# Performance work log

Hardware: AMD Instinct MI355X
Metric: run time of the kernel (lower is better)

Reference implementation:

```python
import jax, jax.numpy as jnp
import numpy as np

GROUPS = 32
EPS = 1e-5


def group_norm(x, scale, bias):
    # x: [B,H,W,C]; stats over (H, W, channels-within-group)
    B, H, W, C = x.shape
    xg = x.reshape(B, H, W, GROUPS, C // GROUPS)
    mean = xg.mean(axis=(1, 2, 4), keepdims=True)
    var = xg.var(axis=(1, 2, 4), keepdims=True)
    xn = ((xg - mean) * jax.lax.rsqrt(var + EPS)).reshape(B, H, W, C)
    return xn * scale + bias


def conv1x1(x, w, b):
    # 1x1 conv == per-pixel matmul; w: [C_in, C_out]
    return jnp.einsum('bhwc,cd->bhwd', x, w) + b


def setup_inputs() -> dict:
    key = jax.random.key(0)
    ks = jax.random.split(key, 10)
    B, H, W, C = 8, 64, 64, 512
    bound = np.sqrt(3.0 / C)  # variance_scaling(1.0, fan_in, uniform)
    x = jax.random.normal(ks[0], (B, H, W, C), dtype=jnp.float32)
    wq = jax.random.uniform(ks[1], (C, C), jnp.float32, -bound, bound)
    wk = jax.random.uniform(ks[2], (C, C), jnp.float32, -bound, bound)
    wv = jax.random.uniform(ks[3], (C, C), jnp.float32, -bound, bound)
    wp = jnp.zeros((C, C), jnp.float32)  # proj_out init scale=0.0
    bq = jnp.zeros((C,), jnp.float32)
    bk = jnp.zeros((C,), jnp.float32)
    bv = jnp.zeros((C,), jnp.float32)
    bp = jnp.zeros((C,), jnp.float32)
    gn_scale = jnp.ones((C,), jnp.float32)
    gn_bias = jnp.zeros((C,), jnp.float32)
    return {"x": x, "wq": wq, "bq": bq, "wk": wk, "bk": bk, "wv": wv,
            "bv": bv, "wp": wp, "bp": bp, "gn_scale": gn_scale, "gn_bias": gn_bias}


def reference(x, wq, bq, wk, bk, wv, bv, wp, bp, gn_scale, gn_bias):
    B, H, W, C = x.shape
    h = group_norm(x, gn_scale, gn_bias)
    q = conv1x1(h, wq, bq).reshape(B, H * W, C)
    k = conv1x1(h, wk, bk).reshape(B, H * W, C)
    v = conv1x1(h, wv, bv).reshape(B, H * W, C)
    # contraction over spatial dim j=H*W -> channel attention [B, C, C]
    attn = jnp.einsum('bji,bjk->bik', q, k)
    attn = jax.nn.softmax(attn, axis=-1)
    h = jnp.einsum('bij,bkj->bik', v, attn)  # [B, HW, C]
    h = h.reshape(B, H, W, C)
    h = conv1x1(h, wp, bp)
    return x + h
```

## Files before the change

kernel.cpp:

```cpp
#include <hip/hip_runtime.h>
#include <hip/hip_bf16.h>


using bf16   = __bf16;
using bf16x8 = __attribute__((ext_vector_type(8))) __bf16;
using bf16x4 = __attribute__((ext_vector_type(4))) __bf16;
using f32x4  = __attribute__((ext_vector_type(4))) float;

#define DI __device__ __forceinline__

DI void gload16(const bf16* g, bf16* l) {
  __builtin_amdgcn_global_load_lds(
      (const __attribute__((address_space(1))) void*)g,
      (__attribute__((address_space(3))) void*)l, 16, 0, 0);
}

DI void gemm128_core(const bf16* __restrict__ A, long lda,
                     const bf16* __restrict__ B, long ldb,
                     int ksteps, bf16* As, bf16* Bs, f32x4 acc[4][4]) {
  const int tid  = threadIdx.x;
  const int lane = tid & 63;
  const int w    = tid >> 6;
  const int lr   = lane & 15;
  const int lk   = (lane >> 4) * 8;
  const int wr   = (w >> 1) * 64;
  const int wc   = (w & 1) * 64;
  const int sw   = (lr & 7) << 3;

  const int  srow = lane >> 3;
  const int  ssw  = ((lane & 7) ^ srow) << 3;
  const bf16* ga = A + (long)(w * 8 + srow) * lda + ssw;
  const bf16* gb = B + (long)(w * 8 + srow) * ldb + ssw;
  bf16* lA = As + w * 512;
  bf16* lB = Bs + w * 512;

  for (int kt = 0; kt < ksteps; ++kt) {
#pragma unroll
    for (int c = 0; c < 4; ++c) {
      gload16(ga + (long)c * 32 * lda, lA + c * 2048);
      gload16(gb + (long)c * 32 * ldb, lB + c * 2048);
    }
    ga += 64; gb += 64;
    __syncthreads();
#pragma unroll
    for (int kk = 0; kk < 2; ++kk) {
      bf16x8 af[4], bfr[4];
#pragma unroll
      for (int i = 0; i < 4; ++i)
        af[i] = *(const bf16x8*)(As + (wr + i * 16 + lr) * 64 + ((kk * 32 + lk) ^ sw));
#pragma unroll
      for (int i = 0; i < 4; ++i)
        bfr[i] = *(const bf16x8*)(Bs + (wc + i * 16 + lr) * 64 + ((kk * 32 + lk) ^ sw));
#pragma unroll
      for (int i = 0; i < 4; ++i)
#pragma unroll
        for (int j = 0; j < 4; ++j)
          acc[i][j] = __builtin_amdgcn_mfma_f32_16x16x32_bf16(af[i], bfr[j], acc[i][j], 0, 0, 0);
    }
    __syncthreads();
  }
}

DI void gemm128x64_core(const bf16* __restrict__ A, long lda,
                        const bf16* __restrict__ B, long ldb,
                        int ksteps, bf16* As, bf16* Bs, f32x4 acc[4][2]) {
  const int tid  = threadIdx.x;
  const int lane = tid & 63;
  const int w    = tid >> 6;
  const int lr   = lane & 15;
  const int lk   = (lane >> 4) * 8;
  const int wr   = (w >> 1) * 64;
  const int wc   = (w & 1) * 32;
  const int sw   = (lr & 7) << 3;

  const int  srow = lane >> 3;
  const int  ssw  = ((lane & 7) ^ srow) << 3;
  const bf16* ga = A + (long)(w * 8 + srow) * lda + ssw;
  const bf16* gb = B + (long)(w * 8 + srow) * ldb + ssw;
  bf16* lA = As + w * 512;
  bf16* lB = Bs + w * 512;

  for (int kt = 0; kt < ksteps; ++kt) {
#pragma unroll
    for (int c = 0; c < 4; ++c)
      gload16(ga + (long)c * 32 * lda, lA + c * 2048);
#pragma unroll
    for (int c = 0; c < 2; ++c)
      gload16(gb + (long)c * 32 * ldb, lB + c * 2048);
    ga += 64; gb += 64;
    __syncthreads();
#pragma unroll
    for (int kk = 0; kk < 2; ++kk) {
      bf16x8 af[4], bfr[2];
#pragma unroll
      for (int i = 0; i < 4; ++i)
        af[i] = *(const bf16x8*)(As + (wr + i * 16 + lr) * 64 + ((kk * 32 + lk) ^ sw));
#pragma unroll
      for (int j = 0; j < 2; ++j)
        bfr[j] = *(const bf16x8*)(Bs + (wc + j * 16 + lr) * 64 + ((kk * 32 + lk) ^ sw));
#pragma unroll
      for (int i = 0; i < 4; ++i)
#pragma unroll
        for (int j = 0; j < 2; ++j)
          acc[i][j] = __builtin_amdgcn_mfma_f32_16x16x32_bf16(af[i], bfr[j], acc[i][j], 0, 0, 0);
    }
    __syncthreads();
  }
}

DI void gemm64_core(const bf16* __restrict__ A, long lda,
                    const bf16* __restrict__ B, long ldb,
                    int ksteps, bf16* As, bf16* Bs, f32x4 acc[2][2]) {
  const int tid  = threadIdx.x;
  const int lane = tid & 63;
  const int w    = tid >> 6;
  const int lr   = lane & 15;
  const int lk   = (lane >> 4) * 8;
  const int wr   = (w >> 1) * 32;
  const int wc   = (w & 1) * 32;
  const int sw   = (lr & 7) << 3;

  const int  srow = lane >> 3;
  const int  ssw  = ((lane & 7) ^ srow) << 3;
  const bf16* ga = A + (long)(w * 8 + srow) * lda + ssw;
  const bf16* gb = B + (long)(w * 8 + srow) * ldb + ssw;
  bf16* lA = As + w * 512;
  bf16* lB = Bs + w * 512;

  for (int kt = 0; kt < ksteps; ++kt) {
#pragma unroll
    for (int c = 0; c < 2; ++c) {
      gload16(ga + (long)c * 32 * lda, lA + c * 2048);
      gload16(gb + (long)c * 32 * ldb, lB + c * 2048);
    }
    ga += 64; gb += 64;
    __syncthreads();
#pragma unroll
    for (int kk = 0; kk < 2; ++kk) {
      bf16x8 af[2], bfr[2];
#pragma unroll
      for (int i = 0; i < 2; ++i)
        af[i] = *(const bf16x8*)(As + (wr + i * 16 + lr) * 64 + ((kk * 32 + lk) ^ sw));
#pragma unroll
      for (int i = 0; i < 2; ++i)
        bfr[i] = *(const bf16x8*)(Bs + (wc + i * 16 + lr) * 64 + ((kk * 32 + lk) ^ sw));
#pragma unroll
      for (int i = 0; i < 2; ++i)
#pragma unroll
        for (int j = 0; j < 2; ++j)
          acc[i][j] = __builtin_amdgcn_mfma_f32_16x16x32_bf16(af[i], bfr[j], acc[i][j], 0, 0, 0);
    }
    __syncthreads();
  }
}

__global__ __launch_bounds__(256) void k_prep(const float* __restrict__ x,
                                              const float* __restrict__ wq,
                                              const float* __restrict__ wk,
                                              const float* __restrict__ wv,
                                              const float* __restrict__ wp,
                                              bf16* __restrict__ WT,
                                              bf16* __restrict__ wvb,
                                              float* __restrict__ s,
                                              float2* __restrict__ stats) {
  __shared__ float shm[1056];
  const int tid = threadIdx.x;
  const int bx = blockIdx.x;
  if (bx < 256) {
    const int b = bx >> 5, g = bx & 31;
    const float* base = x + (size_t)b * 4096 * 512 + g * 16;
    float sm = 0.f, ss = 0.f;
    for (int it = 0; it < 64; ++it) {
      const int idx = it * 256 + tid;
      const int p = idx >> 2, c4 = (idx & 3) * 4;
      float4 v = *(const float4*)(base + (size_t)p * 512 + c4);
      sm += v.x + v.y + v.z + v.w;
      ss += v.x * v.x + v.y * v.y + v.z * v.z + v.w * v.w;
    }
    float* rs = shm; float* rss = shm + 256;
    rs[tid] = sm; rss[tid] = ss; __syncthreads();
    for (int off = 128; off; off >>= 1) {
      if (tid < off) { rs[tid] += rs[tid + off]; rss[tid] += rss[tid + off]; }
      __syncthreads();
    }
    if (tid == 0) {
      float mean = rs[0] * (1.f / 65536.f);
      float var  = rss[0] * (1.f / 65536.f) - mean * mean;
      stats[bx] = float2{mean, rsqrtf(var + 1e-5f)};
    }
  } else {
    const int r = bx - 256;
    const int z = r >> 8;
    const int r2 = r & 255;
    const int bxx = r2 & 15, byy = r2 >> 4;
    const int tx = tid & 31, ty = tid >> 5;
    const float* src = (z == 0) ? wq : (z == 1) ? wk : (z == 2) ? wv : wp;
    const int n0 = bxx * 32, k0 = byy * 32;
    if (z == 0 && byy == 0) s[bxx * 256 + tid] = 0.f;
#pragma unroll
    for (int j = 0; j < 4; ++j) {
      const float v = src[(size_t)(k0 + ty + j * 8) * 512 + n0 + tx];
      shm[(ty + j * 8) * 33 + tx] = v;
      if (z == 2) wvb[(size_t)(k0 + ty + j * 8) * 512 + n0 + tx] = (bf16)v;
    }
    __syncthreads();
#pragma unroll
    for (int j = 0; j < 4; ++j)
      WT[(size_t)(z * 512 + n0 + ty + j * 8) * 512 + k0 + tx] = (bf16)shm[tx * 33 + ty + j * 8];
  }
}

__global__ __launch_bounds__(256) void k_gnapply_t(const float* __restrict__ x,
                                                   const float2* __restrict__ stats,
                                                   const float* __restrict__ gns,
                                                   const float* __restrict__ gnb,
                                                   bf16* __restrict__ Hn,
                                                   bf16* __restrict__ HnT,
                                                   float* __restrict__ s) {
  __shared__ bf16 tile[64 * 516];
  __shared__ float cs[512];
  const int tid = threadIdx.x;
  const int blk = blockIdx.x;
  const int b = blk >> 6, p0 = (blk & 63) * 64;
  cs[tid] = 0.f; cs[tid + 256] = 0.f;
  __syncthreads();

  const int c4 = (tid & 127) * 4;
  const int hi = tid >> 7;
  const float2 st = stats[b * 32 + (c4 >> 4)];
  const float4 sc = *(const float4*)(gns + c4);
  const float4 bi = *(const float4*)(gnb + c4);
  float a0 = 0.f, a1 = 0.f, a2 = 0.f, a3 = 0.f;
  for (int i = 0; i < 32; ++i) {
    const int px = i * 2 + hi;
    const float4 xv = *(const float4*)(x + ((size_t)(b * 4096 + p0 + px)) * 512 + c4);
    const float h0 = (xv.x - st.x) * st.y * sc.x + bi.x;
    const float h1 = (xv.y - st.x) * st.y * sc.y + bi.y;
    const float h2 = (xv.z - st.x) * st.y * sc.z + bi.z;
    const float h3 = (xv.w - st.x) * st.y * sc.w + bi.w;
    a0 += h0; a1 += h1; a2 += h2; a3 += h3;
    bf16x4 hv;
    hv[0] = (bf16)h0; hv[1] = (bf16)h1; hv[2] = (bf16)h2; hv[3] = (bf16)h3;
    *(bf16x4*)(Hn + ((size_t)(b * 4096 + p0 + px)) * 512 + c4) = hv;
    *(bf16x4*)(tile + px * 516 + c4) = hv;
  }
  atomicAdd(&cs[c4 + 0], a0); atomicAdd(&cs[c4 + 1], a1);
  atomicAdd(&cs[c4 + 2], a2); atomicAdd(&cs[c4 + 3], a3);
  __syncthreads();
  atomicAdd(s + b * 512 + tid, cs[tid]);
  atomicAdd(s + b * 512 + 256 + tid, cs[tid + 256]);

  for (int cg = 0; cg < 16; ++cg) {
    const int c  = cg * 32 + (tid >> 3);
    const int so = (tid & 7) * 8;
    bf16x8 pk;
#pragma unroll
    for (int k = 0; k < 8; ++k) pk[k] = tile[(so + k) * 516 + c];
    *(bf16x8*)(HnT + ((size_t)(b * 512 + c)) * 4096 + p0 + so) = pk;
  }
}

__global__ __launch_bounds__(256) void k_gram(const bf16* __restrict__ HnT,
                                              bf16* __restrict__ part) {
  __shared__ bf16 As[128 * 64], Bs[128 * 64];
  const int Lb = blockIdx.x;
  const int b  = Lb & 7;
  const int idx = Lb >> 3;
  const int sp = idx & 3;
  const int t  = idx >> 2;
  const int m0 = (int)((0x3221110000ull >> (4 * t)) & 15) * 128;
  const int n0 = (int)((0x3323213210ull >> (4 * t)) & 15) * 128;
  f32x4 acc[4][4];
#pragma unroll
  for (int i = 0; i < 4; ++i)
#pragma unroll
    for (int j = 0; j < 4; ++j) acc[i][j] = (f32x4){0.f, 0.f, 0.f, 0.f};
  const bf16* A = HnT + ((size_t)b * 512 + m0) * 4096 + sp * 1024;
  const bf16* B = HnT + ((size_t)b * 512 + n0) * 4096 + sp * 1024;
  gemm128_core(A, 4096, B, 4096, 16, As, Bs, acc);

  const int lane = threadIdx.x & 63, w = threadIdx.x >> 6;
  const int wr = (w >> 1) * 64, wc = (w & 1) * 64;
  const int rr = (lane >> 4) * 4, cc = lane & 15;
  bf16* dst = part + (size_t)(sp * 8 + b) * 262144;
#pragma unroll
  for (int i = 0; i < 4; ++i) {
#pragma unroll
    for (int j = 0; j < 4; ++j) {
      const int gm = m0 + wr + i * 16 + rr;
      const int gn = n0 + wc + j * 16 + cc;
      bf16* p = dst + (size_t)gm * 512 + gn;
      p[0]    = (bf16)acc[i][j][0];
      p[512]  = (bf16)acc[i][j][1];
      p[1024] = (bf16)acc[i][j][2];
      p[1536] = (bf16)acc[i][j][3];
      if (m0 != n0) {
        bf16x4 pk;
        pk[0] = (bf16)acc[i][j][0]; pk[1] = (bf16)acc[i][j][1];
        pk[2] = (bf16)acc[i][j][2]; pk[3] = (bf16)acc[i][j][3];
        *(bf16x4*)(dst + (size_t)gn * 512 + gm) = pk;
      }
    }
  }
}

__global__ __launch_bounds__(256) void k_gsumv(const bf16* __restrict__ part,
                                               bf16* __restrict__ G,
                                               const bf16* __restrict__ WT,
                                               const float* __restrict__ s,
                                               float* __restrict__ uq,
                                               float* __restrict__ vkv) {
  const int bx = blockIdx.x, tid = threadIdx.x;
  if (bx < 2048) {
    const size_t S8 = (size_t)8 * 262144;
    const size_t i4 = ((size_t)bx * 256 + tid) * 4;
    const bf16x4 a = *(const bf16x4*)(part + i4);
    const bf16x4 c = *(const bf16x4*)(part + i4 + S8);
    const bf16x4 d = *(const bf16x4*)(part + i4 + 2 * S8);
    const bf16x4 e = *(const bf16x4*)(part + i4 + 3 * S8);
    bf16x4 o;
#pragma unroll
    for (int j = 0; j < 4; ++j)
      o[j] = (bf16)((float)a[j] + (float)c[j] + (float)d[j] + (float)e[j]);
    *(bf16x4*)(G + i4) = o;
  } else {
    const int z = bx - 2048;
    const int which = z >> 3, b = z & 7;
    const float* sv = s + b * 512;
    for (int o = tid; o < 512; o += 256) {
      const bf16* row = WT + ((size_t)(which * 512 + o)) * 512;
      float acc = 0.f;
      for (int c = 0; c < 512; c += 8) {
        bf16x8 v = *(const bf16x8*)(row + c);
        const float4 s0 = *(const float4*)(sv + c);
        const float4 s1 = *(const float4*)(sv + c + 4);
        acc += (float)v[0] * s0.x + (float)v[1] * s0.y + (float)v[2] * s0.z +
               (float)v[3] * s0.w + (float)v[4] * s1.x + (float)v[5] * s1.y +
               (float)v[6] * s1.z + (float)v[7] * s1.w;
      }
      (which == 0 ? uq : vkv)[b * 512 + o] = acc;
    }
  }
}

__global__ __launch_bounds__(256) void k_sg64_bf(const bf16* __restrict__ Ab, long a_bs,
                                                 const bf16* __restrict__ Bb, long b_bs,
                                                 bf16* __restrict__ Cb) {
  __shared__ bf16 As[64 * 64], Bs[64 * 64];
  const int b = blockIdx.z;
  const int m0 = blockIdx.y * 64, n0 = blockIdx.x * 64;
  f32x4 acc[2][2];
#pragma unroll
  for (int i = 0; i < 2; ++i)
#pragma unroll
    for (int j = 0; j < 2; ++j) acc[i][j] = (f32x4){0.f, 0.f, 0.f, 0.f};
  gemm64_core(Ab + (size_t)b * a_bs + (size_t)m0 * 512, 512,
              Bb + (size_t)b * b_bs + (size_t)n0 * 512, 512, 8, As, Bs, acc);

  const int lane = threadIdx.x & 63, w = threadIdx.x >> 6;
  const int wr = (w >> 1) * 32, wc = (w & 1) * 32;
  const int rr = (lane >> 4) * 4, cc = lane & 15;
  bf16* dst = Cb + (size_t)b * 262144;
#pragma unroll
  for (int i = 0; i < 2; ++i) {
#pragma unroll
    for (int j = 0; j < 2; ++j) {
      const int gm = m0 + wr + i * 16 + rr;
      const int gn = n0 + wc + j * 16 + cc;
      bf16* p = dst + (size_t)gm * 512 + gn;
      p[0]    = (bf16)acc[i][j][0];
      p[512]  = (bf16)acc[i][j][1];
      p[1024] = (bf16)acc[i][j][2];
      p[1536] = (bf16)acc[i][j][3];
    }
  }
}

__global__ __launch_bounds__(256) void k_sgT(const bf16* __restrict__ WTp,
                                             const bf16* __restrict__ attnT,
                                             bf16* __restrict__ T,
                                             const float* __restrict__ attnbv,
                                             float* __restrict__ dv) {
  const int tid = threadIdx.x;
  if (blockIdx.z == 8) {
    __shared__ float abvs[512];
    __shared__ float dvp[64][4];
    const int b = blockIdx.y, n0 = blockIdx.x * 64;
    for (int c = tid; c < 512; c += 256) abvs[c] = attnbv[b * 512 + c];
    __syncthreads();
    const int o = tid & 63, q = tid >> 6;
    const bf16* wrow = WTp + (size_t)(n0 + o) * 512 + q * 128;
    float acc = 0.f;
#pragma unroll
    for (int kk = 0; kk < 16; ++kk) {
      bf16x8 v = *(const bf16x8*)(wrow + kk * 8);
#pragma unroll
      for (int j = 0; j < 8; ++j) acc += (float)v[j] * abvs[q * 128 + kk * 8 + j];
    }
    dvp[o][q] = acc;
    __syncthreads();
    if (tid < 64)
      dv[b * 512 + n0 + tid] = dvp[tid][0] + dvp[tid][1] + dvp[tid][2] + dvp[tid][3];
    return;
  }
  __shared__ bf16 As[64 * 64], Bs[64 * 64];
  const int b = blockIdx.z;
  const int m0 = blockIdx.y * 64, n0 = blockIdx.x * 64;
  f32x4 acc[2][2];
#pragma unroll
  for (int i = 0; i < 2; ++i)
#pragma unroll
    for (int j = 0; j < 2; ++j) acc[i][j] = (f32x4){0.f, 0.f, 0.f, 0.f};
  gemm64_core(WTp + (size_t)m0 * 512,
              512, attnT + (size_t)b * 262144 + (size_t)n0 * 512, 512, 8, As, Bs, acc);

  const int lane = tid & 63, w = tid >> 6;
  const int wr = (w >> 1) * 32, wc = (w & 1) * 32;
  const int rr = (lane >> 4) * 4, cc = lane & 15;
  bf16* dst = T + (size_t)b * 262144;
#pragma unroll
  for (int i = 0; i < 2; ++i) {
#pragma unroll
    for (int j = 0; j < 2; ++j) {
      const int gm = m0 + wr + i * 16 + rr;
      const int gn = n0 + wc + j * 16 + cc;
      bf16* p = dst + (size_t)gm * 512 + gn;
      p[0]    = (bf16)acc[i][j][0];
      p[512]  = (bf16)acc[i][j][1];
      p[1024] = (bf16)acc[i][j][2];
      p[1536] = (bf16)acc[i][j][3];
    }
  }
}

__global__ __launch_bounds__(256) void k_sg64_f32(const bf16* __restrict__ Ab, long a_bs,
                                                  const bf16* __restrict__ Bb, long b_bs,
                                                  float* __restrict__ Cb) {
  __shared__ bf16 As[64 * 64], Bs[64 * 64];
  const int b = blockIdx.z;
  const int m0 = blockIdx.y * 64, n0 = blockIdx.x * 64;
  f32x4 acc[2][2];
#pragma unroll
  for (int i = 0; i < 2; ++i)
#pragma unroll
    for (int j = 0; j < 2; ++j) acc[i][j] = (f32x4){0.f, 0.f, 0.f, 0.f};
  gemm64_core(Ab + (size_t)b * a_bs + (size_t)m0 * 512, 512,
              Bb + (size_t)b * b_bs + (size_t)n0 * 512, 512, 8, As, Bs, acc);

  const int lane = threadIdx.x & 63, w = threadIdx.x >> 6;
  const int wr = (w >> 1) * 32, wc = (w & 1) * 32;
  const int rr = (lane >> 4) * 4, cc = lane & 15;
  float* dst = Cb + (size_t)b * 262144;
#pragma unroll
  for (int i = 0; i < 2; ++i) {
#pragma unroll
    for (int j = 0; j < 2; ++j) {
      const int gm = m0 + wr + i * 16 + rr;
      const int gn = n0 + wc + j * 16 + cc;
      float* p = dst + (size_t)gm * 512 + gn;
      p[0]    = acc[i][j][0];
      p[512]  = acc[i][j][1];
      p[1024] = acc[i][j][2];
      p[1536] = acc[i][j][3];
    }
  }
}

__global__ __launch_bounds__(256) void k_smax(const float* __restrict__ L,
                                              const float* __restrict__ uq,
                                              const float* __restrict__ vkv,
                                              const float* __restrict__ bq,
                                              const float* __restrict__ bk,
                                              const float* __restrict__ bv,
                                              bf16* __restrict__ attnT,
                                              float* __restrict__ attnbv) {
  __shared__ bf16 p[4][512];
  const int tid = threadIdx.x;
  const int w = tid >> 6, l = tid & 63;
  const int blk = blockIdx.x;
  const int gr = blk * 4 + w;
  const int b = gr >> 9, i = gr & 511;
  const int c = l * 8;

  const float r  = uq[b * 512 + i];
  const float q0 = bq[i];
  const float* lp = L + (size_t)gr * 512 + c;
  const float4 l0 = *(const float4*)lp;
  const float4 l1 = *(const float4*)(lp + 4);
  const float4 k0 = *(const float4*)(bk + c);
  const float4 k1 = *(const float4*)(bk + c + 4);
  const float4 g0 = *(const float4*)(vkv + b * 512 + c);
  const float4 g1 = *(const float4*)(vkv + b * 512 + c + 4);
  float v[8];
  v[0] = l0.x + r * k0.x + q0 * (g0.x + 4096.f * k0.x);
  v[1] = l0.y + r * k0.y + q0 * (g0.y + 4096.f * k0.y);
  v[2] = l0.z + r * k0.z + q0 * (g0.z + 4096.f * k0.z);
  v[3] = l0.w + r * k0.w + q0 * (g0.w + 4096.f * k0.w);
  v[4] = l1.x + r * k1.x + q0 * (g1.x + 4096.f * k1.x);
  v[5] = l1.y + r * k1.y + q0 * (g1.y + 4096.f * k1.y);
  v[6] = l1.z + r * k1.z + q0 * (g1.z + 4096.f * k1.z);
  v[7] = l1.w + r * k1.w + q0 * (g1.w + 4096.f * k1.w);

  float mx = v[0];
#pragma unroll
  for (int j = 1; j < 8; ++j) mx = fmaxf(mx, v[j]);
  for (int off = 32; off; off >>= 1) mx = fmaxf(mx, __shfl_xor(mx, off));
  float e[8], sm = 0.f;
#pragma unroll
  for (int j = 0; j < 8; ++j) { e[j] = __expf(v[j] - mx); sm += e[j]; }
  for (int off = 32; off; off >>= 1) sm += __shfl_xor(sm, off);
  const float inv = 1.f / sm;

  const float4 b0 = *(const float4*)(bv + c);
  const float4 b1 = *(const float4*)(bv + c + 4);
  float ab = e[0] * b0.x + e[1] * b0.y + e[2] * b0.z + e[3] * b0.w +
             e[4] * b1.x + e[5] * b1.y + e[6] * b1.z + e[7] * b1.w;
  ab *= inv;
  for (int off = 32; off; off >>= 1) ab += __shfl_xor(ab, off);
  if (l == 0) attnbv[gr] = ab;

  bf16x8 o;
#pragma unroll
  for (int j = 0; j < 8; ++j) o[j] = (bf16)(e[j] * inv);
  *(bf16x8*)(&p[w][c]) = o;
  __syncthreads();

  const int i0 = (blk * 4) & 511;
  for (int n = tid; n < 512; n += 256) {
    bf16x4 t;
    t[0] = p[0][n]; t[1] = p[1][n]; t[2] = p[2][n]; t[3] = p[3][n];
    *(bf16x4*)(attnT + (size_t)b * 262144 + (size_t)n * 512 + i0) = t;
  }
}

__global__ __launch_bounds__(256) void k_final(const bf16* __restrict__ Hn,
                                               const bf16* __restrict__ CT,
                                               const float* __restrict__ dv,
                                               const float* __restrict__ bp,
                                               const float* __restrict__ x,
                                               float* __restrict__ out) {
  __shared__ bf16 As[128 * 64], Bs[64 * 64];
  const int Lb = blockIdx.x;
  const int b  = Lb & 7;
  const int idx = Lb >> 3;
  const int m0 = (idx >> 3) * 128;
  const int n0 = (idx & 7) * 64;
  const int tid = threadIdx.x;

  f32x4 acc[4][2];
#pragma unroll
  for (int i = 0; i < 4; ++i)
#pragma unroll
    for (int j = 0; j < 2; ++j) acc[i][j] = (f32x4){0.f, 0.f, 0.f, 0.f};
  gemm128x64_core(Hn + ((size_t)(b * 4096 + m0)) * 512, 512,
                  CT + (size_t)b * 262144 + (size_t)n0 * 512, 512, 8, As, Bs, acc);

  const int lane = tid & 63, w = tid >> 6;
  const int wr = (w >> 1) * 64, wc = (w & 1) * 32;
  const int rr = (lane >> 4) * 4, cc = lane & 15;
#pragma unroll
  for (int i = 0; i < 4; ++i) {
#pragma unroll
    for (int j = 0; j < 2; ++j) {
      const int gm = m0 + wr + i * 16 + rr;
      const int gn = n0 + wc + j * 16 + cc;
      const float add = dv[b * 512 + gn] + bp[gn];
#pragma unroll
      for (int jj = 0; jj < 4; ++jj) {
        const size_t off = ((size_t)(b * 4096 + gm + jj)) * 512 + gn;
        out[off] = acc[i][j][jj] + add + x[off];
      }
    }
  }
}

extern "C" void kernel_launch(void* const* d_in, const int* in_sizes, int n_in,
                              void* d_out, int out_size, void* d_ws, size_t ws_size,
                              hipStream_t stream) {
  const float* x   = (const float*)d_in[0];
  const float* wq  = (const float*)d_in[1];
  const float* bq  = (const float*)d_in[2];
  const float* wk  = (const float*)d_in[3];
  const float* bk  = (const float*)d_in[4];
  const float* wv  = (const float*)d_in[5];
  const float* bv  = (const float*)d_in[6];
  const float* wp  = (const float*)d_in[7];
  const float* bp  = (const float*)d_in[8];
  const float* gns = (const float*)d_in[9];
  const float* gnb = (const float*)d_in[10];
  float* out = (float*)d_out;

  const size_t MB = 1ull << 20;
  const size_t KB = 1024;
  char* wsb = (char*)d_ws;
  bf16*   WT     = (bf16*)(wsb);
  bf16*   wvb    = (bf16*)(wsb + 2 * MB);
  float2* stats  = (float2*)(wsb + 2 * MB + 512 * KB);
  float*  s      = (float*)(wsb + 2 * MB + 576 * KB);
  float*  uq     = (float*)(wsb + 2 * MB + 640 * KB);
  float*  vkv    = (float*)(wsb + 2 * MB + 704 * KB);
  float*  dv     = (float*)(wsb + 2 * MB + 768 * KB);
  float*  attnbv = (float*)(wsb + 2 * MB + 832 * KB);
  bf16*   Hn     = (bf16*)(wsb + 3 * MB);
  bf16*   HnT    = (bf16*)(wsb + 35 * MB);
  bf16*   part   = (bf16*)(wsb + 67 * MB);
  bf16*   attnT  = (bf16*)(wsb + 67 * MB);
  bf16*   T      = (bf16*)(wsb + 71 * MB);
  bf16*   CT     = (bf16*)(wsb + 75 * MB);
  bf16*   G      = (bf16*)(wsb + 99 * MB);
  bf16*   M1     = (bf16*)(wsb + 103 * MB);
  float*  L      = (float*)(wsb + 107 * MB);

  const long S2 = 512 * 512;

  k_prep      <<<dim3(1280),    dim3(256), 0, stream>>>(x, wq, wk, wv, wp, WT, wvb, s, stats);
  k_gnapply_t <<<dim3(512),     dim3(256), 0, stream>>>(x, stats, gns, gnb, Hn, HnT, s);
  k_gram      <<<dim3(320),     dim3(256), 0, stream>>>(HnT, part);
  k_gsumv     <<<dim3(2064),    dim3(256), 0, stream>>>(part, G, WT, s, uq, vkv);
  k_sg64_bf   <<<dim3(8, 8, 8), dim3(256), 0, stream>>>(WT, 0, G, S2, M1);
  k_sg64_f32  <<<dim3(8, 8, 8), dim3(256), 0, stream>>>(M1, S2, WT + (size_t)512 * 512, 0, L);
  k_smax      <<<dim3(1024),    dim3(256), 0, stream>>>(L, uq, vkv, bq, bk, bv, attnT, attnbv);
  k_sgT       <<<dim3(8, 8, 9), dim3(256), 0, stream>>>(WT + (size_t)3 * 512 * 512, attnT, T,
                                                        attnbv, dv);
  k_sg64_bf   <<<dim3(8, 8, 8), dim3(256), 0, stream>>>(T, S2, wvb, 0, CT);
  k_final     <<<dim3(2048),    dim3(256), 0, stream>>>(Hn, CT, dv, bp, x, out);
}
```

Baseline: 163.7 us.

## Fuse chained 512x512 GEMMs with softmax into two row-block kernels

Replaces the separate M1 GEMM, logits GEMM and softmax kernels with one kernel that computes a 64-row slab of Wq·G in shared memory, multiplies by Wk, and applies bias terms and softmax in registers before writing attnT. A second kernel does the same for the T = Wp·attn and CT = T·Wv chain, keeping T in LDS. This drops the M1, L and T global round trips and three launches. In exchange it launches only 64 and 128 blocks with large LDS (~136KB) and heavy register use, so occupancy and per-CU parallelism fall sharply.

Measured after the change: 197.0 us. +20.4%, slower.

```diff
diff --git a/kernel.cpp b/kernel.cpp
--- a/kernel.cpp
+++ b/kernel.cpp
@@ -100,52 +100,6 @@
         bfr[j] = *(const bf16x8*)(Bs + (wc + j * 16 + lr) * 64 + ((kk * 32 + lk) ^ sw));
 #pragma unroll
       for (int i = 0; i < 4; ++i)
-#pragma unroll
-        for (int j = 0; j < 2; ++j)
-          acc[i][j] = __builtin_amdgcn_mfma_f32_16x16x32_bf16(af[i], bfr[j], acc[i][j], 0, 0, 0);
-    }
-    __syncthreads();
-  }
-}
-
-DI void gemm64_core(const bf16* __restrict__ A, long lda,
-                    const bf16* __restrict__ B, long ldb,
-                    int ksteps, bf16* As, bf16* Bs, f32x4 acc[2][2]) {
-  const int tid  = threadIdx.x;
-  const int lane = tid & 63;
-  const int w    = tid >> 6;
-  const int lr   = lane & 15;
-  const int lk   = (lane >> 4) * 8;
-  const int wr   = (w >> 1) * 32;
-  const int wc   = (w & 1) * 32;
-  const int sw   = (lr & 7) << 3;
-
-  const int  srow = lane >> 3;
-  const int  ssw  = ((lane & 7) ^ srow) << 3;
-  const bf16* ga = A + (long)(w * 8 + srow) * lda + ssw;
-  const bf16* gb = B + (long)(w * 8 + srow) * ldb + ssw;
-  bf16* lA = As + w * 512;
-  bf16* lB = Bs + w * 512;
-
-  for (int kt = 0; kt < ksteps; ++kt) {
-#pragma unroll
-    for (int c = 0; c < 2; ++c) {
-      gload16(ga + (long)c * 32 * lda, lA + c * 2048);
-      gload16(gb + (long)c * 32 * ldb, lB + c * 2048);
-    }
-    ga += 64; gb += 64;
-    __syncthreads();
-#pragma unroll
-    for (int kk = 0; kk < 2; ++kk) {
-      bf16x8 af[2], bfr[2];
-#pragma unroll
-      for (int i = 0; i < 2; ++i)
-        af[i] = *(const bf16x8*)(As + (wr + i * 16 + lr) * 64 + ((kk * 32 + lk) ^ sw));
-#pragma unroll
-      for (int i = 0; i < 2; ++i)
-        bfr[i] = *(const bf16x8*)(Bs + (wc + i * 16 + lr) * 64 + ((kk * 32 + lk) ^ sw));
-#pragma unroll
-      for (int i = 0; i < 2; ++i)
 #pragma unroll
         for (int j = 0; j < 2; ++j)
           acc[i][j] = __builtin_amdgcn_mfma_f32_16x16x32_bf16(af[i], bfr[j], acc[i][j], 0, 0, 0);
@@ -343,49 +297,187 @@
   }
 }
 
-__global__ __launch_bounds__(256) void k_sg64_bf(const bf16* __restrict__ Ab, long a_bs,
-                                                 const bf16* __restrict__ Bb, long b_bs,
-                                                 bf16* __restrict__ Cb) {
-  __shared__ bf16 As[64 * 64], Bs[64 * 64];
-  const int b = blockIdx.z;
-  const int m0 = blockIdx.y * 64, n0 = blockIdx.x * 64;
-  f32x4 acc[2][2];
-#pragma unroll
-  for (int i = 0; i < 2; ++i)
-#pragma unroll
-    for (int j = 0; j < 2; ++j) acc[i][j] = (f32x4){0.f, 0.f, 0.f, 0.f};
-  gemm64_core(Ab + (size_t)b * a_bs + (size_t)m0 * 512, 512,
-              Bb + (size_t)b * b_bs + (size_t)n0 * 512, 512, 8, As, Bs, acc);
-
-  const int lane = threadIdx.x & 63, w = threadIdx.x >> 6;
-  const int wr = (w >> 1) * 32, wc = (w & 1) * 32;
-  const int rr = (lane >> 4) * 4, cc = lane & 15;
-  bf16* dst = Cb + (size_t)b * 262144;
-#pragma unroll
-  for (int i = 0; i < 2; ++i) {
-#pragma unroll
-    for (int j = 0; j < 2; ++j) {
-      const int gm = m0 + wr + i * 16 + rr;
-      const int gn = n0 + wc + j * 16 + cc;
-      bf16* p = dst + (size_t)gm * 512 + gn;
-      p[0]    = (bf16)acc[i][j][0];
-      p[512]  = (bf16)acc[i][j][1];
-      p[1024] = (bf16)acc[i][j][2];
-      p[1536] = (bf16)acc[i][j][3];
-    }
-  }
-}
-
-__global__ __launch_bounds__(256) void k_sgT(const bf16* __restrict__ WTp,
+__global__ __launch_bounds__(256) void k_lsm(const bf16* __restrict__ WT,
+                                             const bf16* __restrict__ G,
+                                             const float* __restrict__ uq,
+                                             const float* __restrict__ vkv,
+                                             const float* __restrict__ bq,
+                                             const float* __restrict__ bk,
+                                             const float* __restrict__ bv,
+                                             bf16* __restrict__ attnT,
+                                             float* __restrict__ attnbv) {
+  __shared__ __align__(16) bf16 Bp[512 * 64];
+  __shared__ __align__(16) bf16 Ap[64 * 64];
+  __shared__ __align__(16) bf16 M1s[64 * 512];
+  __shared__ float w2s[512], bks[512], bvs[512], uqs[64], bqs[64];
+  const int tid = threadIdx.x;
+  const int lane = tid & 63, w = tid >> 6;
+  const int b = blockIdx.x & 7, m0 = (blockIdx.x >> 3) * 64;
+  const bf16* WTq = WT;
+  const bf16* WTk = WT + (size_t)262144;
+  const bf16* Gb  = G + (size_t)b * 262144;
+
+  for (int c = tid; c < 512; c += 256) {
+    const float bkc = bk[c];
+    bks[c] = bkc;
+    w2s[c] = vkv[b * 512 + c] + 4096.f * bkc;
+    bvs[c] = bv[c];
+  }
+  if (tid < 64) { uqs[tid] = uq[b * 512 + m0 + tid]; bqs[tid] = bq[m0 + tid]; }
+
+  const int lr = lane & 15;
+  const int g  = lane >> 4;
+  const int lk = g * 8;
+  const int sw = (lr & 7) << 3;
+  const int srow = lane >> 3;
+  const int ssw  = ((lane & 7) ^ srow) << 3;
+
+  const bf16* gA = WTq + (size_t)(m0 + w * 8 + srow) * 512 + ssw;
+  const bf16* gB = Gb + (size_t)(w * 8 + srow) * 512 + ssw;
+  bf16* lA = Ap + w * 512;
+  bf16* lB = Bp + w * 512;
+
+  f32x4 acc[8][4];
+#pragma unroll
+  for (int t = 0; t < 8; ++t)
+#pragma unroll
+    for (int mi = 0; mi < 4; ++mi) acc[t][mi] = (f32x4){0.f, 0.f, 0.f, 0.f};
+  for (int kt = 0; kt < 8; ++kt) {
+#pragma unroll
+    for (int c = 0; c < 2; ++c)
+      gload16(gA + (size_t)(c * 32) * 512 + kt * 64, lA + c * 2048);
+#pragma unroll
+    for (int c = 0; c < 16; ++c)
+      gload16(gB + (size_t)(c * 32) * 512 + kt * 64, lB + c * 2048);
+    __syncthreads();
+#pragma unroll
+    for (int kk = 0; kk < 2; ++kk) {
+      bf16x8 bfm[4];
+#pragma unroll
+      for (int mi = 0; mi < 4; ++mi)
+        bfm[mi] = *(const bf16x8*)(Ap + (mi * 16 + lr) * 64 + ((kk * 32 + lk) ^ sw));
+#pragma unroll
+      for (int t = 0; t < 8; ++t) {
+        bf16x8 af = *(const bf16x8*)(Bp + (w * 128 + t * 16 + lr) * 64 + ((kk * 32 + lk) ^ sw));
+#pragma unroll
+        for (int mi = 0; mi < 4; ++mi)
+          acc[t][mi] = __builtin_amdgcn_mfma_f32_16x16x32_bf16(af, bfm[mi], acc[t][mi], 0, 0, 0);
+      }
+    }
+    __syncthreads();
+  }
+#pragma unroll
+  for (int t = 0; t < 8; ++t)
+#pragma unroll
+    for (int mi = 0; mi < 4; ++mi) {
+      const int m  = mi * 16 + lr;
+      const int k2 = w * 128 + t * 16 + g * 4;
+      const int col8s = (((k2 & 63) >> 3) ^ (m & 7));
+      bf16x4 pk;
+      pk[0] = (bf16)acc[t][mi][0]; pk[1] = (bf16)acc[t][mi][1];
+      pk[2] = (bf16)acc[t][mi][2]; pk[3] = (bf16)acc[t][mi][3];
+      *(bf16x4*)(M1s + m * 512 + (k2 >> 6) * 64 + col8s * 8 + (k2 & 7)) = pk;
+    }
+  __syncthreads();
+
+  f32x4 acc2[32];
+#pragma unroll
+  for (int t = 0; t < 32; ++t) acc2[t] = (f32x4){0.f, 0.f, 0.f, 0.f};
+  const bf16* gB2 = WTk + (size_t)(w * 8 + srow) * 512 + ssw;
+  for (int kt = 0; kt < 8; ++kt) {
+#pragma unroll
+    for (int c = 0; c < 16; ++c)
+      gload16(gB2 + (size_t)(c * 32) * 512 + kt * 64, lB + c * 2048);
+    __syncthreads();
+#pragma unroll
+    for (int kk = 0; kk < 2; ++kk) {
+      bf16x8 af = *(const bf16x8*)(M1s + (w * 16 + lr) * 512 + kt * 64 +
+                                   (((kk * 4 + g) ^ (lr & 7)) * 8));
+#pragma unroll
+      for (int t = 0; t < 32; ++t) {
+        bf16x8 bfr = *(const bf16x8*)(Bp + (t * 16 + lr) * 64 + ((kk * 32 + lk) ^ sw));
+        acc2[t] = __builtin_amdgcn_mfma_f32_16x16x32_bf16(af, bfr, acc2[t], 0, 0, 0);
+      }
+    }
+    __syncthreads();
+  }
+
+  float uql[4], bql[4];
+#pragma unroll
+  for (int r = 0; r < 4; ++r) {
+    uql[r] = uqs[w * 16 + g * 4 + r];
+    bql[r] = bqs[w * 16 + g * 4 + r];
+  }
+#pragma unroll
+  for (int t = 0; t < 32; ++t) {
+    const int n = t * 16 + lr;
+    const float bkn = bks[n], w2n = w2s[n];
+#pragma unroll
+    for (int r = 0; r < 4; ++r)
+      acc2[t][r] += uql[r] * bkn + bql[r] * w2n;
+  }
+  float mx[4] = {-3.4e38f, -3.4e38f, -3.4e38f, -3.4e38f};
+#pragma unroll
+  for (int t = 0; t < 32; ++t)
+#pragma unroll
+    for (int r = 0; r < 4; ++r) mx[r] = fmaxf(mx[r], acc2[t][r]);
+#pragma unroll
+  for (int off = 1; off < 16; off <<= 1)
+#pragma unroll
+    for (int r = 0; r < 4; ++r) mx[r] = fmaxf(mx[r], __shfl_xor(mx[r], off));
+  float sm[4] = {0.f, 0.f, 0.f, 0.f}, ab[4] = {0.f, 0.f, 0.f, 0.f};
+#pragma unroll
+  for (int t = 0; t < 32; ++t) {
+    const int n = t * 16 + lr;
+    const float bvn = bvs[n];
+#pragma unroll
+    for (int r = 0; r < 4; ++r) {
+      const float e = __expf(acc2[t][r] - mx[r]);
+      acc2[t][r] = e;
+      sm[r] += e;
+      ab[r] += e * bvn;
+    }
+  }
+#pragma unroll
+  for (int off = 1; off < 16; off <<= 1)
+#pragma unroll
+    for (int r = 0; r < 4; ++r) {
+      sm[r] += __shfl_xor(sm[r], off);
+      ab[r] += __shfl_xor(ab[r], off);
+    }
+  float inv[4];
+#pragma unroll
+  for (int r = 0; r < 4; ++r) inv[r] = 1.f / sm[r];
+  if (lr == 0) {
+#pragma unroll
+    for (int r = 0; r < 4; ++r)
+      attnbv[b * 512 + m0 + w * 16 + g * 4 + r] = ab[r] * inv[r];
+  }
+#pragma unroll
+  for (int t = 0; t < 32; ++t) {
+    const int n = t * 16 + lr;
+    bf16x4 pk;
+#pragma unroll
+    for (int r = 0; r < 4; ++r) pk[r] = (bf16)(acc2[t][r] * inv[r]);
+    *(bf16x4*)(attnT + (size_t)b * 262144 + (size_t)n * 512 + m0 + w * 16 + g * 4) = pk;
+  }
+}
+
+__global__ __launch_bounds__(256) void k_tct(const bf16* __restrict__ WTp,
                                              const bf16* __restrict__ attnT,
-                                             bf16* __restrict__ T,
+                                             const bf16* __restrict__ wvb,
                                              const float* __restrict__ attnbv,
+                                             bf16* __restrict__ CT,
                                              float* __restrict__ dv) {
+  __shared__ __align__(16) bf16 Bp[512 * 64];
+  __shared__ __align__(16) bf16 Ap[64 * 64];
+  __shared__ __align__(16) bf16 Ts[64 * 512];
+  __shared__ float dvp[64][4];
   const int tid = threadIdx.x;
-  if (blockIdx.z == 8) {
-    __shared__ float abvs[512];
-    __shared__ float dvp[64][4];
-    const int b = blockIdx.y, n0 = blockIdx.x * 64;
+  if (blockIdx.x >= 64) {
+    float* abvs = (float*)Ap;
+    const int z = blockIdx.x - 64;
+    const int b = z & 7, n0 = (z >> 3) * 64;
     for (int c = tid; c < 512; c += 256) abvs[c] = attnbv[b * 512 + c];
     __syncthreads();
     const int o = tid & 63, q = tid >> 6;
@@ -403,133 +495,93 @@
       dv[b * 512 + n0 + tid] = dvp[tid][0] + dvp[tid][1] + dvp[tid][2] + dvp[tid][3];
     return;
   }
-  __shared__ bf16 As[64 * 64], Bs[64 * 64];
-  const int b = blockIdx.z;
-  const int m0 = blockIdx.y * 64, n0 = blockIdx.x * 64;
-  f32x4 acc[2][2];
-#pragma unroll
-  for (int i = 0; i < 2; ++i)
-#pragma unroll
-    for (int j = 0; j < 2; ++j) acc[i][j] = (f32x4){0.f, 0.f, 0.f, 0.f};
-  gemm64_core(WTp + (size_t)m0 * 512,
-              512, attnT + (size_t)b * 262144 + (size_t)n0 * 512, 512, 8, As, Bs, acc);
-
   const int lane = tid & 63, w = tid >> 6;
-  const int wr = (w >> 1) * 32, wc = (w & 1) * 32;
-  const int rr = (lane >> 4) * 4, cc = lane & 15;
-  bf16* dst = T + (size_t)b * 262144;
-#pragma unroll
-  for (int i = 0; i < 2; ++i) {
-#pragma unroll
-    for (int j = 0; j < 2; ++j) {
-      const int gm = m0 + wr + i * 16 + rr;
-      const int gn = n0 + wc + j * 16 + cc;
-      bf16* p = dst + (size_t)gm * 512 + gn;
-      p[0]    = (bf16)acc[i][j][0];
-      p[512]  = (bf16)acc[i][j][1];
-      p[1024] = (bf16)acc[i][j][2];
-      p[1536] = (bf16)acc[i][j][3];
-    }
-  }
-}
-
-__global__ __launch_bounds__(256) void k_sg64_f32(const bf16* __restrict__ Ab, long a_bs,
-                                                  const bf16* __restrict__ Bb, long b_bs,
-                                                  float* __restrict__ Cb) {
-  __shared__ bf16 As[64 * 64], Bs[64 * 64];
-  const int b = blockIdx.z;
-  const int m0 = blockIdx.y * 64, n0 = blockIdx.x * 64;
-  f32x4 acc[2][2];
-#pragma unroll
-  for (int i = 0; i < 2; ++i)
-#pragma unroll
-    for (int j = 0; j < 2; ++j) acc[i][j] = (f32x4){0.f, 0.f, 0.f, 0.f};
-  gemm64_core(Ab + (size_t)b * a_bs + (size_t)m0 * 512, 512,
-              Bb + (size_t)b * b_bs + (size_t)n0 * 512, 512, 8, As, Bs, acc);
-
-  const int lane = threadIdx.x & 63, w = threadIdx.x >> 6;
-  const int wr = (w >> 1) * 32, wc = (w & 1) * 32;
-  const int rr = (lane >> 4) * 4, cc = lane & 15;
-  float* dst = Cb + (size_t)b * 262144;
-#pragma unroll
-  for (int i = 0; i < 2; ++i) {
-#pragma unroll
-    for (int j = 0; j < 2; ++j) {
-      const int gm = m0 + wr + i * 16 + rr;
-      const int gn = n0 + wc + j * 16 + cc;
-      float* p = dst + (size_t)gm * 512 + gn;
-      p[0]    = acc[i][j][0];
-      p[512]  = acc[i][j][1];
-      p[1024] = acc[i][j][2];
-      p[1536] = acc[i][j][3];
-    }
-  }
-}
-
-__global__ __launch_bounds__(256) void k_smax(const float* __restrict__ L,
-                                              const float* __restrict__ uq,
-                                              const float* __restrict__ vkv,
-                                              const float* __restrict__ bq,
-                                              const float* __restrict__ bk,
-                                              const float* __restrict__ bv,
-                                              bf16* __restrict__ attnT,
-                                              float* __restrict__ attnbv) {
-  __shared__ bf16 p[4][512];
-  const int tid = threadIdx.x;
-  const int w = tid >> 6, l = tid & 63;
-  const int blk = blockIdx.x;
-  const int gr = blk * 4 + w;
-  const int b = gr >> 9, i = gr & 511;
-  const int c = l * 8;
-
-  const float r  = uq[b * 512 + i];
-  const float q0 = bq[i];
-  const float* lp = L + (size_t)gr * 512 + c;
-  const float4 l0 = *(const float4*)lp;
-  const float4 l1 = *(const float4*)(lp + 4);
-  const float4 k0 = *(const float4*)(bk + c);
-  const float4 k1 = *(const float4*)(bk + c + 4);
-  const float4 g0 = *(const float4*)(vkv + b * 512 + c);
-  const float4 g1 = *(const float4*)(vkv + b * 512 + c + 4);
-  float v[8];
-  v[0] = l0.x + r * k0.x + q0 * (g0.x + 4096.f * k0.x);
-  v[1] = l0.y + r * k0.y + q0 * (g0.y + 4096.f * k0.y);
-  v[2] = l0.z + r * k0.z + q0 * (g0.z + 4096.f * k0.z);
-  v[3] = l0.w + r * k0.w + q0 * (g0.w + 4096.f * k0.w);
-  v[4] = l1.x + r * k1.x + q0 * (g1.x + 4096.f * k1.x);
-  v[5] = l1.y + r * k1.y + q0 * (g1.y + 4096.f * k1.y);
-  v[6] = l1.z + r * k1.z + q0 * (g1.z + 4096.f * k1.z);
-  v[7] = l1.w + r * k1.w + q0 * (g1.w + 4096.f * k1.w);
-
-  float mx = v[0];
-#pragma unroll
-  for (int j = 1; j < 8; ++j) mx = fmaxf(mx, v[j]);
-  for (int off = 32; off; off >>= 1) mx = fmaxf(mx, __shfl_xor(mx, off));
-  float e[8], sm = 0.f;
-#pragma unroll
-  for (int j = 0; j < 8; ++j) { e[j] = __expf(v[j] - mx); sm += e[j]; }
-  for (int off = 32; off; off >>= 1) sm += __shfl_xor(sm, off);
-  const float inv = 1.f / sm;
-
-  const float4 b0 = *(const float4*)(bv + c);
-  const float4 b1 = *(const float4*)(bv + c + 4);
-  float ab = e[0] * b0.x + e[1] * b0.y + e[2] * b0.z + e[3] * b0.w +
-             e[4] * b1.x + e[5] * b1.y + e[6] * b1.z + e[7] * b1.w;
-  ab *= inv;
-  for (int off = 32; off; off >>= 1) ab += __shfl_xor(ab, off);
-  if (l == 0) attnbv[gr] = ab;
-
-  bf16x8 o;
-#pragma unroll
-  for (int j = 0; j < 8; ++j) o[j] = (bf16)(e[j] * inv);
-  *(bf16x8*)(&p[w][c]) = o;
+  const int b = blockIdx.x & 7, m0 = (blockIdx.x >> 3) * 64;
+  const bf16* Ab = attnT + (size_t)b * 262144;
+
+  const int lr = lane & 15;
+  const int g  = lane >> 4;
+  const int lk = g * 8;
+  const int sw = (lr & 7) << 3;
+  const int srow = lane >> 3;
+  const int ssw  = ((lane & 7) ^ srow) << 3;
+
+  const bf16* gA = WTp + (size_t)(m0 + w * 8 + srow) * 512 + ssw;
+  const bf16* gB = Ab + (size_t)(w * 8 + srow) * 512 + ssw;
+  bf16* lA = Ap + w * 512;
+  bf16* lB = Bp + w * 512;
+
+  f32x4 acc[8][4];
+#pragma unroll
+  for (int t = 0; t < 8; ++t)
+#pragma unroll
+    for (int mi = 0; mi < 4; ++mi) acc[t][mi] = (f32x4){0.f, 0.f, 0.f, 0.f};
+  for (int kt = 0; kt < 8; ++kt) {
+#pragma unroll
+    for (int c = 0; c < 2; ++c)
+      gload16(gA + (size_t)(c * 32) * 512 + kt * 64, lA + c * 2048);
+#pragma unroll
+    for (int c = 0; c < 16; ++c)
+      gload16(gB + (size_t)(c * 32) * 512 + kt * 64, lB + c * 2048);
+    __syncthreads();
+#pragma unroll
+    for (int kk = 0; kk < 2; ++kk) {
+      bf16x8 bfm[4];
+#pragma unroll
+      for (int mi = 0; mi < 4; ++mi)
+        bfm[mi] = *(const bf16x8*)(Ap + (mi * 16 + lr) * 64 + ((kk * 32 + lk) ^ sw));
+#pragma unroll
+      for (int t = 0; t < 8; ++t) {
+        bf16x8 af = *(const bf16x8*)(Bp + (w * 128 + t * 16 + lr) * 64 + ((kk * 32 + lk) ^ sw));
+#pragma unroll
+        for (int mi = 0; mi < 4; ++mi)
+          acc[t][mi] = __builtin_amdgcn_mfma_f32_16x16x32_bf16(af, bfm[mi], acc[t][mi], 0, 0, 0);
+      }
+    }
+    __syncthreads();
+  }
+#pragma unroll
+  for (int t = 0; t < 8; ++t)
+#pragma unroll
+    for (int mi = 0; mi < 4; ++mi) {
+      const int m = mi * 16 + lr;
+      const int n = w * 128 + t * 16 + g * 4;
+      const int col8s = (((n & 63) >> 3) ^ (m & 7));
+      bf16x4 pk;
+      pk[0] = (bf16)acc[t][mi][0]; pk[1] = (bf16)acc[t][mi][1];
+      pk[2] = (bf16)acc[t][mi][2]; pk[3] = (bf16)acc[t][mi][3];
+      *(bf16x4*)(Ts + m * 512 + (n >> 6) * 64 + col8s * 8 + (n & 7)) = pk;
+    }
   __syncthreads();
 
-  const int i0 = (blk * 4) & 511;
-  for (int n = tid; n < 512; n += 256) {
-    bf16x4 t;
-    t[0] = p[0][n]; t[1] = p[1][n]; t[2] = p[2][n]; t[3] = p[3][n];
-    *(bf16x4*)(attnT + (size_t)b * 262144 + (size_t)n * 512 + i0) = t;
+  f32x4 acc2[32];
+#pragma unroll
+  for (int t = 0; t < 32; ++t) acc2[t] = (f32x4){0.f, 0.f, 0.f, 0.f};
+  const bf16* gB2 = wvb + (size_t)(w * 8 + srow) * 512 + ssw;
+  for (int kt = 0; kt < 8; ++kt) {
+#pragma unroll
+    for (int c = 0; c < 16; ++c)
+      gload16(gB2 + (size_t)(c * 32) * 512 + kt * 64, lB + c * 2048);
+    __syncthreads();
+#pragma unroll
+    for (int kk = 0; kk < 2; ++kk) {
+      bf16x8 af = *(const bf16x8*)(Ts + (w * 16 + lr) * 512 + kt * 64 +
+                                   (((kk * 4 + g) ^ (lr & 7)) * 8));
+#pragma unroll
+      for (int t = 0; t < 32; ++t) {
+        bf16x8 bfr = *(const bf16x8*)(Bp + (t * 16 + lr) * 64 + ((kk * 32 + lk) ^ sw));
+        acc2[t] = __builtin_amdgcn_mfma_f32_16x16x32_bf16(af, bfr, acc2[t], 0, 0, 0);
+      }
+    }
+    __syncthreads();
+  }
+  bf16* dst = CT + (size_t)b * 262144;
+#pragma unroll
+  for (int t = 0; t < 32; ++t) {
+    const int n = t * 16 + lr;
+#pragma unroll
+    for (int r = 0; r < 4; ++r)
+      dst[(size_t)(m0 + w * 16 + g * 4 + r) * 512 + n] = (bf16)acc2[t][r];
   }
 }
 
@@ -605,23 +657,15 @@
   bf16*   HnT    = (bf16*)(wsb + 35 * MB);
   bf16*   part   = (bf16*)(wsb + 67 * MB);
   bf16*   attnT  = (bf16*)(wsb + 67 * MB);
-  bf16*   T      = (bf16*)(wsb + 71 * MB);
   bf16*   CT     = (bf16*)(wsb + 75 * MB);
   bf16*   G      = (bf16*)(wsb + 99 * MB);
-  bf16*   M1     = (bf16*)(wsb + 103 * MB);
-  float*  L      = (float*)(wsb + 107 * MB);
-
-  const long S2 = 512 * 512;
-
-  k_prep      <<<dim3(1280),    dim3(256), 0, stream>>>(x, wq, wk, wv, wp, WT, wvb, s, stats);
-  k_gnapply_t <<<dim3(512),     dim3(256), 0, stream>>>(x, stats, gns, gnb, Hn, HnT, s);
-  k_gram      <<<dim3(320),     dim3(256), 0, stream>>>(HnT, part);
-  k_gsumv     <<<dim3(2064),    dim3(256), 0, stream>>>(part, G, WT, s, uq, vkv);
-  k_sg64_bf   <<<dim3(8, 8, 8), dim3(256), 0, stream>>>(WT, 0, G, S2, M1);
-  k_sg64_f32  <<<dim3(8, 8, 8), dim3(256), 0, stream>>>(M1, S2, WT + (size_t)512 * 512, 0, L);
-  k_smax      <<<dim3(1024),    dim3(256), 0, stream>>>(L, uq, vkv, bq, bk, bv, attnT, attnbv);
-  k_sgT       <<<dim3(8, 8, 9), dim3(256), 0, stream>>>(WT + (size_t)3 * 512 * 512, attnT, T,
-                                                        attnbv, dv);
-  k_sg64_bf   <<<dim3(8, 8, 8), dim3(256), 0, stream>>>(T, S2, wvb, 0, CT);
-  k_final     <<<dim3(2048),    dim3(256), 0, stream>>>(Hn, CT, dv, bp, x, out);
-}
+
+  k_prep      <<<dim3(1280), dim3(256), 0, stream>>>(x, wq, wk, wv, wp, WT, wvb, s, stats);
+  k_gnapply_t <<<dim3(512),  dim3(256), 0, stream>>>(x, stats, gns, gnb, Hn, HnT, s);
+  k_gram      <<<dim3(320),  dim3(256), 0, stream>>>(HnT, part);
+  k_gsumv     <<<dim3(2064), dim3(256), 0, stream>>>(part, G, WT, s, uq, vkv);
+  k_lsm       <<<dim3(64),   dim3(256), 0, stream>>>(WT, G, uq, vkv, bq, bk, bv, attnT, attnbv);
+  k_tct       <<<dim3(128),  dim3(256), 0, stream>>>(WT + (size_t)3 * 262144, attnT, wvb,
+                                                     attnbv, CT, dv);
+  k_final     <<<dim3(2048), dim3(256), 0, stream>>>(Hn, CT, dv, bp, x, out);
+}
```

## Recompute group-norm in final GEMM instead of storing Hn

Applied to the files above, without the earlier changes.

Drops the bf16 Hn buffer written by the group-norm apply kernel. The final GEMM now reads fp32 x directly, applies per-channel group-norm scale and shift from shared memory, converts to bf16 and writes the swizzled A tile into LDS. This removes a 32 MB write and a 32 MB read of Hn. In exchange, each final-GEMM block reads fp32 x, which is twice the bytes of Hn and is read once per N tile. The A-tile loads also become synchronous register loads rather than async global-to-LDS copies.

New measurement: 176.3 us. 1.08x slower.

```diff
diff --git a/kernel.cpp b/kernel.cpp
--- a/kernel.cpp
+++ b/kernel.cpp
@@ -55,53 +55,6 @@
       for (int i = 0; i < 4; ++i)
 #pragma unroll
         for (int j = 0; j < 4; ++j)
-          acc[i][j] = __builtin_amdgcn_mfma_f32_16x16x32_bf16(af[i], bfr[j], acc[i][j], 0, 0, 0);
-    }
-    __syncthreads();
-  }
-}
-
-DI void gemm128x64_core(const bf16* __restrict__ A, long lda,
-                        const bf16* __restrict__ B, long ldb,
-                        int ksteps, bf16* As, bf16* Bs, f32x4 acc[4][2]) {
-  const int tid  = threadIdx.x;
-  const int lane = tid & 63;
-  const int w    = tid >> 6;
-  const int lr   = lane & 15;
-  const int lk   = (lane >> 4) * 8;
-  const int wr   = (w >> 1) * 64;
-  const int wc   = (w & 1) * 32;
-  const int sw   = (lr & 7) << 3;
-
-  const int  srow = lane >> 3;
-  const int  ssw  = ((lane & 7) ^ srow) << 3;
-  const bf16* ga = A + (long)(w * 8 + srow) * lda + ssw;
-  const bf16* gb = B + (long)(w * 8 + srow) * ldb + ssw;
-  bf16* lA = As + w * 512;
-  bf16* lB = Bs + w * 512;
-
-  for (int kt = 0; kt < ksteps; ++kt) {
-#pragma unroll
-    for (int c = 0; c < 4; ++c)
-      gload16(ga + (long)c * 32 * lda, lA + c * 2048);
-#pragma unroll
-    for (int c = 0; c < 2; ++c)
-      gload16(gb + (long)c * 32 * ldb, lB + c * 2048);
-    ga += 64; gb += 64;
-    __syncthreads();
-#pragma unroll
-    for (int kk = 0; kk < 2; ++kk) {
-      bf16x8 af[4], bfr[2];
-#pragma unroll
-      for (int i = 0; i < 4; ++i)
-        af[i] = *(const bf16x8*)(As + (wr + i * 16 + lr) * 64 + ((kk * 32 + lk) ^ sw));
-#pragma unroll
-      for (int j = 0; j < 2; ++j)
-        bfr[j] = *(const bf16x8*)(Bs + (wc + j * 16 + lr) * 64 + ((kk * 32 + lk) ^ sw));
-#pragma unroll
-      for (int i = 0; i < 4; ++i)
-#pragma unroll
-        for (int j = 0; j < 2; ++j)
           acc[i][j] = __builtin_amdgcn_mfma_f32_16x16x32_bf16(af[i], bfr[j], acc[i][j], 0, 0, 0);
     }
     __syncthreads();
@@ -214,7 +167,6 @@
                                                    const float2* __restrict__ stats,
                                                    const float* __restrict__ gns,
                                                    const float* __restrict__ gnb,
-                                                   bf16* __restrict__ Hn,
                                                    bf16* __restrict__ HnT,
                                                    float* __restrict__ s) {
   __shared__ bf16 tile[64 * 516];
@@ -241,7 +193,6 @@
     a0 += h0; a1 += h1; a2 += h2; a3 += h3;
     bf16x4 hv;
     hv[0] = (bf16)h0; hv[1] = (bf16)h1; hv[2] = (bf16)h2; hv[3] = (bf16)h3;
-    *(bf16x4*)(Hn + ((size_t)(b * 4096 + p0 + px)) * 512 + c4) = hv;
     *(bf16x4*)(tile + px * 516 + c4) = hv;
   }
   atomicAdd(&cs[c4 + 0], a0); atomicAdd(&cs[c4 + 1], a1);
@@ -533,13 +484,16 @@
   }
 }
 
-__global__ __launch_bounds__(256) void k_final(const bf16* __restrict__ Hn,
+__global__ __launch_bounds__(256) void k_final(const float* __restrict__ x,
+                                               const float2* __restrict__ stats,
+                                               const float* __restrict__ gns,
+                                               const float* __restrict__ gnb,
                                                const bf16* __restrict__ CT,
                                                const float* __restrict__ dv,
                                                const float* __restrict__ bp,
-                                               const float* __restrict__ x,
                                                float* __restrict__ out) {
   __shared__ bf16 As[128 * 64], Bs[64 * 64];
+  __shared__ float gsc[512], gbs[512];
   const int Lb = blockIdx.x;
   const int b  = Lb & 7;
   const int idx = Lb >> 3;
@@ -547,16 +501,72 @@
   const int n0 = (idx & 7) * 64;
   const int tid = threadIdx.x;
 
+  for (int c = tid; c < 512; c += 256) {
+    const float2 st = stats[b * 32 + (c >> 4)];
+    const float a = st.y * gns[c];
+    gsc[c] = a;
+    gbs[c] = gnb[c] - st.x * a;
+  }
+  __syncthreads();
+
+  const int lane = tid & 63, w = tid >> 6;
+  const int lr = lane & 15, lk = (lane >> 4) * 8;
+  const int wr = (w >> 1) * 64, wc = (w & 1) * 32;
+  const int sw = (lr & 7) << 3;
+  const int srow = lane >> 3;
+  const int ssw  = ((lane & 7) ^ srow) << 3;
+  const bf16* gb = CT + (size_t)b * 262144 + (size_t)(n0 + w * 8 + srow) * 512 + ssw;
+  bf16* lB = Bs + w * 512;
+
   f32x4 acc[4][2];
 #pragma unroll
   for (int i = 0; i < 4; ++i)
 #pragma unroll
     for (int j = 0; j < 2; ++j) acc[i][j] = (f32x4){0.f, 0.f, 0.f, 0.f};
-  gemm128x64_core(Hn + ((size_t)(b * 4096 + m0)) * 512, 512,
-                  CT + (size_t)b * 262144 + (size_t)n0 * 512, 512, 8, As, Bs, acc);
-
-  const int lane = tid & 63, w = tid >> 6;
-  const int wr = (w >> 1) * 64, wc = (w & 1) * 32;
+
+  for (int kt = 0; kt < 8; ++kt) {
+#pragma unroll
+    for (int c2 = 0; c2 < 2; ++c2)
+      gload16(gb + (size_t)(c2 * 32) * 512, lB + c2 * 2048);
+    gb += 64;
+#pragma unroll
+    for (int c2 = 0; c2 < 4; ++c2) {
+      const int idx2 = c2 * 256 + tid;
+      const int row = idx2 >> 3;
+      const int ch0 = kt * 64 + (idx2 & 7) * 8;
+      const float* xp = x + ((size_t)(b * 4096 + m0 + row)) * 512 + ch0;
+      const float4 x0 = *(const float4*)xp;
+      const float4 x1 = *(const float4*)(xp + 4);
+      bf16x8 hv;
+      hv[0] = (bf16)(x0.x * gsc[ch0 + 0] + gbs[ch0 + 0]);
+      hv[1] = (bf16)(x0.y * gsc[ch0 + 1] + gbs[ch0 + 1]);
+      hv[2] = (bf16)(x0.z * gsc[ch0 + 2] + gbs[ch0 + 2]);
+      hv[3] = (bf16)(x0.w * gsc[ch0 + 3] + gbs[ch0 + 3]);
+      hv[4] = (bf16)(x1.x * gsc[ch0 + 4] + gbs[ch0 + 4]);
+      hv[5] = (bf16)(x1.y * gsc[ch0 + 5] + gbs[ch0 + 5]);
+      hv[6] = (bf16)(x1.z * gsc[ch0 + 6] + gbs[ch0 + 6]);
+      hv[7] = (bf16)(x1.w * gsc[ch0 + 7] + gbs[ch0 + 7]);
+      *(bf16x8*)(As + row * 64 + (((idx2 & 7) ^ (row & 7)) * 8)) = hv;
+    }
+    __syncthreads();
+#pragma unroll
+    for (int kk = 0; kk < 2; ++kk) {
+      bf16x8 af[4], bfr[2];
+#pragma unroll
+      for (int i = 0; i < 4; ++i)
+        af[i] = *(const bf16x8*)(As + (wr + i * 16 + lr) * 64 + ((kk * 32 + lk) ^ sw));
+#pragma unroll
+      for (int j = 0; j < 2; ++j)
+        bfr[j] = *(const bf16x8*)(Bs + (wc + j * 16 + lr) * 64 + ((kk * 32 + lk) ^ sw));
+#pragma unroll
+      for (int i = 0; i < 4; ++i)
+#pragma unroll
+        for (int j = 0; j < 2; ++j)
+          acc[i][j] = __builtin_amdgcn_mfma_f32_16x16x32_bf16(af[i], bfr[j], acc[i][j], 0, 0, 0);
+    }
+    __syncthreads();
+  }
+
   const int rr = (lane >> 4) * 4, cc = lane & 15;
 #pragma unroll
   for (int i = 0; i < 4; ++i) {
@@ -601,7 +611,6 @@
   float*  vkv    = (float*)(wsb + 2 * MB + 704 * KB);
   float*  dv     = (float*)(wsb + 2 * MB + 768 * KB);
   float*  attnbv = (float*)(wsb + 2 * MB + 832 * KB);
-  bf16*   Hn     = (bf16*)(wsb + 3 * MB);
   bf16*   HnT    = (bf16*)(wsb + 35 * MB);
   bf16*   part   = (bf16*)(wsb + 67 * MB);
   bf16*   attnT  = (bf16*)(wsb + 67 * MB);
@@ -614,7 +623,7 @@
   const long S2 = 512 * 512;
 
   k_prep      <<<dim3(1280),    dim3(256), 0, stream>>>(x, wq, wk, wv, wp, WT, wvb, s, stats);
-  k_gnapply_t <<<dim3(512),     dim3(256), 0, stream>>>(x, stats, gns, gnb, Hn, HnT, s);
+  k_gnapply_t <<<dim3(512),     dim3(256), 0, stream>>>(x, stats, gns, gnb, HnT, s);
   k_gram      <<<dim3(320),     dim3(256), 0, stream>>>(HnT, part);
   k_gsumv     <<<dim3(2064),    dim3(256), 0, stream>>>(part, G, WT, s, uq, vkv);
   k_sg64_bf   <<<dim3(8, 8, 8), dim3(256), 0, stream>>>(WT, 0, G, S2, M1);
@@ -623,5 +632,5 @@
   k_sgT       <<<dim3(8, 8, 9), dim3(256), 0, stream>>>(WT + (size_t)3 * 512 * 512, attnT, T,
                                                         attnbv, dv);
   k_sg64_bf   <<<dim3(8, 8, 8), dim3(256), 0, stream>>>(T, S2, wvb, 0, CT);
-  k_final     <<<dim3(2048),    dim3(256), 0, stream>>>(Hn, CT, dv, bp, x, out);
-}
+  k_final     <<<dim3(2048),    dim3(256), 0, stream>>>(x, stats, gns, gnb, CT, dv, bp, out);
+}
```
